# Optimization experiments

Hardware: AMD Instinct MI355X
Metric: run time of the kernel (lower is better)

## Reference

```python
import jax, jax.numpy as jnp
import numpy as np

LEAKY = 0.1

def _leaky(x):
    return jax.nn.leaky_relu(x, LEAKY)

def _gather(pts, idx):
    # pts: [B, M, C], idx: [B, N, K] -> [B, N, K, C]
    return jax.vmap(lambda p, i: p[i])(pts, idx)

def _cross(xyz1, xyz2, p1, p2, pos_w, pos_b, mlps, k):
    # xyz1:[B,N1,3] xyz2:[B,N2,3] p1:[B,N1,D] p2:[B,N2,D]
    d = (jnp.sum(xyz1 * xyz1, -1)[:, :, None]
         + jnp.sum(xyz2 * xyz2, -1)[:, None, :]
         - 2.0 * jnp.einsum('bnc,bmc->bnm', xyz1, xyz2))  # [B,N1,N2]
    _, idx = jax.lax.top_k(-d, k)                          # smallest-k -> [B,N1,K]
    nb_xyz = _gather(xyz2, idx)                            # [B,N1,K,3]
    direction = nb_xyz - xyz1[:, :, None, :]
    g2 = _gather(p2, idx)                                  # [B,N1,K,D]
    posf = direction @ pos_w.T + pos_b                     # 1x1 conv on 3->D
    x = _leaky(g2 + p1[:, :, None, :] + posf)              # bn = Identity
    for w, b in mlps:
        x = _leaky(x @ w.T + b)                            # 1x1 Conv2d + bias + leaky
    return jnp.max(x, axis=2)                              # max-pool over K -> [B,N1,Cout]

def setup_inputs() -> dict:
    key = jax.random.key(0)
    ks = jax.random.split(key, 24)
    B, N, C, M1, M2, K = 2, 8192, 64, 64, 64, 16
    s = 0.1
    inp = {
        'pc1': jax.random.normal(ks[0], (B, 3, N), jnp.float32),
        'pc2': jax.random.normal(ks[1], (B, 3, N), jnp.float32),
        'feat1': jax.random.normal(ks[2], (B, C, N), jnp.float32),
        'feat2': jax.random.normal(ks[3], (B, C, N), jnp.float32),
        't11_w': jax.random.normal(ks[4], (M1, C), jnp.float32) * s,
        't11_b': jax.random.normal(ks[5], (M1,), jnp.float32) * s,
        't22_w': jax.random.normal(ks[6], (M1, C), jnp.float32) * s,
        't22_b': jax.random.normal(ks[7], (M1,), jnp.float32) * s,
        'pos1_w': jax.random.normal(ks[8], (M1, 3), jnp.float32) * s,
        'pos1_b': jax.random.normal(ks[9], (M1,), jnp.float32) * s,
        'mlp1_w1': jax.random.normal(ks[10], (M1, M1), jnp.float32) * s,
        'mlp1_b1': jax.random.normal(ks[11], (M1,), jnp.float32) * s,
        'mlp1_w2': jax.random.normal(ks[12], (M1, M1), jnp.float32) * s,
        'mlp1_b2': jax.random.normal(ks[13], (M1,), jnp.float32) * s,
        't1_w': jax.random.normal(ks[14], (M2, M1), jnp.float32) * s,
        't1_b': jax.random.normal(ks[15], (M2,), jnp.float32) * s,
        't2_w': jax.random.normal(ks[16], (M2, M1), jnp.float32) * s,
        't2_b': jax.random.normal(ks[17], (M2,), jnp.float32) * s,
        'pos2_w': jax.random.normal(ks[18], (M2, 3), jnp.float32) * s,
        'pos2_b': jax.random.normal(ks[19], (M2,), jnp.float32) * s,
        'mlp2_w1': jax.random.normal(ks[20], (M2, M2), jnp.float32) * s,
        'mlp2_b1': jax.random.normal(ks[21], (M2,), jnp.float32) * s,
    }
    return inp

def reference(pc1, pc2, feat1, feat2,
              t11_w, t11_b, t22_w, t22_b,
              pos1_w, pos1_b, mlp1_w1, mlp1_b1, mlp1_w2, mlp1_b2,
              t1_w, t1_b, t2_w, t2_b,
              pos2_w, pos2_b, mlp2_w1, mlp2_b1):
    K = 16
    x1 = jnp.transpose(pc1, (0, 2, 1))    # [B,N,3]
    x2 = jnp.transpose(pc2, (0, 2, 1))
    f1 = jnp.transpose(feat1, (0, 2, 1))  # [B,N,C]
    f2 = jnp.transpose(feat2, (0, 2, 1))
    mlp1 = [(mlp1_w1, mlp1_b1), (mlp1_w2, mlp1_b2)]
    mlp2 = [(mlp2_w1, mlp2_b1)]
    # feat1_new = cross_t1(cross(pc1, pc2, t11(feat1), t22(feat2), pos1, mlp1))
    q1 = f1 @ t11_w.T + t11_b
    q2 = f2 @ t22_w.T + t22_b
    fn1 = _cross(x1, x2, q1, q2, pos1_w, pos1_b, mlp1, K) @ t1_w.T + t1_b  # [B,N,M2]
    # feat2_new = cross_t2(cross(pc2, pc1, t11(feat2), t22(feat1), pos1, mlp1))
    r1 = f2 @ t11_w.T + t11_b
    r2 = f1 @ t22_w.T + t22_b
    fn2 = _cross(x2, x1, r1, r2, pos1_w, pos1_b, mlp1, K) @ t2_w.T + t2_b  # [B,N,M2]
    # feat1_final = cross(pc1, pc2, feat1_new, feat2_new, pos2, mlp2)
    ff = _cross(x1, x2, fn1, fn2, pos2_w, pos2_b, mlp2, K)                 # [B,N,M2]
    to_cn = lambda a: jnp.transpose(a, (0, 2, 1))  # back to [B,C,N] torch layout
    return (to_cn(fn1), to_cn(fn2), to_cn(ff))
```

## Files before the change

kernel.cpp:

```cpp
#include <hip/hip_runtime.h>

#define NPTS 8192
#define BATCH 2
#define CC 64
#define KNN 16

typedef __attribute__((ext_vector_type(4))) float  f32x4;
typedef __attribute__((ext_vector_type(8))) short  s16x8;
typedef unsigned short u16;

__device__ __forceinline__ u16 f2bf(float f) {
  unsigned u = __float_as_uint(f);
  unsigned r = ((u >> 16) & 1u) + 0x7FFFu;
  return (u16)((u + r) >> 16);
}

__device__ __forceinline__ float leaky(float v) { return fmaxf(v, 0.1f * v); }

__device__ __forceinline__ s16x8 pack8(const float v[8]) {
  union { s16x8 v8; u16 s[8]; } u;
  #pragma unroll
  for (int j = 0; j < 8; ++j) u.s[j] = f2bf(v[j]);
  return u.v8;
}

__device__ __forceinline__ void split2(float v, u16& h, u16& l) {
  h = f2bf(v);
  float hf = __uint_as_float((unsigned)h << 16);
  l = f2bf(v - hf);
}

__global__ __launch_bounds__(256) void kprep(const float* __restrict__ pc1,
                                             const float* __restrict__ pc2,
                                             float4* __restrict__ x1t,
                                             float4* __restrict__ x2t,
                                             u16* __restrict__ arow1, u16* __restrict__ arow2,
                                             u16* __restrict__ brow1, u16* __restrict__ brow2) {
  int i = blockIdx.x * 256 + threadIdx.x;
  int b = i >> 13, n = i & (NPTS - 1);
  size_t base = (size_t)b * 3 * NPTS + n;
  #pragma unroll
  for (int c = 0; c < 2; ++c) {
    const float* pc = c ? pc2 : pc1;
    float4* xt = c ? x2t : x1t;
    u16* ar = c ? arow2 : arow1;
    u16* br = c ? brow2 : brow1;
    float x = pc[base], y = pc[base + NPTS], z = pc[base + 2 * NPTS];
    float w = x * x + y * y + z * z;
    xt[i] = make_float4(x, y, z, w);
    u16 A[32];
    #pragma unroll
    for (int j = 0; j < 32; ++j) A[j] = 0;
    u16 h, l;
    split2(-2.f * x, h, l); A[0] = h; A[1] = l; A[2] = h;
    split2(-2.f * y, h, l); A[3] = h; A[4] = l; A[5] = h;
    split2(-2.f * z, h, l); A[6] = h; A[7] = l; A[8] = h;
    split2(w, h, l);        A[9] = h; A[10] = l;
    A[11] = 0x3F80; A[12] = 0x3F80;
    uint4* ap = (uint4*)(ar + (size_t)i * 32);
    ap[0] = ((const uint4*)A)[0];
    ap[1] = ((const uint4*)A)[1];
    ap[2] = ((const uint4*)A)[2];
    ap[3] = ((const uint4*)A)[3];
    u16 Bv[16];
    #pragma unroll
    for (int j = 0; j < 16; ++j) Bv[j] = 0;
    split2(x, h, l); Bv[0] = h; Bv[1] = h; Bv[2] = l;
    split2(y, h, l); Bv[3] = h; Bv[4] = h; Bv[5] = l;
    split2(z, h, l); Bv[6] = h; Bv[7] = h; Bv[8] = l;
    Bv[9] = 0x3F80; Bv[10] = 0x3F80;
    split2(w, h, l); Bv[11] = h; Bv[12] = l;
    uint4* bp = (uint4*)(br + (size_t)i * 16);
    bp[0] = ((const uint4*)Bv)[0];
    bp[1] = ((const uint4*)Bv)[1];
  }
}

__global__ __launch_bounds__(256) void ktrans(
    const float* __restrict__ f1, const float* __restrict__ f2,
    const float* __restrict__ w11, const float* __restrict__ b11,
    const float* __restrict__ w22, const float* __restrict__ b22,
    float* __restrict__ q1, float* __restrict__ q2,
    float* __restrict__ r1, float* __restrict__ r2) {
  const int z = blockIdx.z;
  const float* in = (z == 0 || z == 3) ? f1 : f2;
  const float* W  = (z == 0 || z == 2) ? w11 : w22;
  const float* Bb = (z == 0 || z == 2) ? b11 : b22;
  float* out = (z == 0) ? q1 : (z == 1) ? q2 : (z == 2) ? r1 : r2;
  const int b = blockIdx.y;
  const int n0 = blockIdx.x * 64;
  const int t = threadIdx.x;

  __shared__ float ft[64 * 65];
  __shared__ float wt[64 * 68];

  #pragma unroll
  for (int j = 0; j < 16; ++j) {
    int e = t + 256 * j;
    int c = e >> 6, tn = e & 63;
    ft[c * 65 + tn] = in[((size_t)b * 64 + c) * NPTS + n0 + tn];
  }
  #pragma unroll
  for (int j = 0; j < 16; ++j) {
    int e = t + 256 * j;
    int mm = e >> 6, c = e & 63;
    wt[c * 68 + mm] = W[e];
  }
  __syncthreads();

  const int tn = t & 63, mg = t >> 6;
  float a[16];
  #pragma unroll
  for (int u = 0; u < 4; ++u) {
    float4 bb = *(const float4*)&Bb[16 * mg + 4 * u];
    a[4 * u] = bb.x; a[4 * u + 1] = bb.y; a[4 * u + 2] = bb.z; a[4 * u + 3] = bb.w;
  }
  for (int c = 0; c < 64; ++c) {
    float x = ft[c * 65 + tn];
    #pragma unroll
    for (int u = 0; u < 4; ++u) {
      float4 w4 = *(const float4*)&wt[c * 68 + 16 * mg + 4 * u];
      a[4 * u]     = fmaf(x, w4.x, a[4 * u]);
      a[4 * u + 1] = fmaf(x, w4.y, a[4 * u + 1]);
      a[4 * u + 2] = fmaf(x, w4.z, a[4 * u + 2]);
      a[4 * u + 3] = fmaf(x, w4.w, a[4 * u + 3]);
    }
  }
  size_t ob = ((size_t)b * NPTS + n0 + tn) * 64 + 16 * mg;
  #pragma unroll
  for (int u = 0; u < 4; ++u)
    *(float4*)&out[ob + 4 * u] =
        make_float4(a[4 * u], a[4 * u + 1], a[4 * u + 2], a[4 * u + 3]);
}

__device__ __forceinline__ void kinsert(unsigned key, unsigned ii,
                                        unsigned (&D)[16], unsigned (&I)[16]) {
  if (key < D[15]) {
    bool lt[16];
    #pragma unroll
    for (int j = 0; j < 16; ++j) lt[j] = key < D[j];
    #pragma unroll
    for (int j = 15; j >= 1; --j) {
      D[j] = lt[j - 1] ? D[j - 1] : (lt[j] ? key : D[j]);
      I[j] = lt[j - 1] ? I[j - 1] : (lt[j] ? ii  : I[j]);
    }
    if (lt[0]) { D[0] = key; I[0] = ii; }
  }
}

__device__ __forceinline__ void klex(unsigned key, unsigned ii,
                                     unsigned (&D)[16], unsigned (&I)[16]) {
  if ((key < D[15]) || (key == D[15] && ii < I[15])) {
    bool lt[16];
    #pragma unroll
    for (int j = 0; j < 16; ++j) lt[j] = (key < D[j]) || (key == D[j] && ii < I[j]);
    #pragma unroll
    for (int j = 15; j >= 1; --j) {
      D[j] = lt[j - 1] ? D[j - 1] : (lt[j] ? key : D[j]);
      I[j] = lt[j - 1] ? I[j - 1] : (lt[j] ? ii  : I[j]);
    }
    if (lt[0]) { D[0] = key; I[0] = ii; }
  }
}

#define CH 4
#define CKSZ (NPTS / CH)
#define RD 15
#define RT 11
#define FDELTA 0.008f
#define KINF 0x7F7FFFFFu

__global__ __launch_bounds__(256) void kknn(
    const float4* __restrict__ x1t, const float4* __restrict__ x2t,
    const u16* __restrict__ arow1, const u16* __restrict__ arow2,
    const u16* __restrict__ brow1, const u16* __restrict__ brow2,
    uint2* __restrict__ part) {
  const int dir = blockIdx.z;
  const int b = blockIdx.y;
  const float4* xq = dir ? x2t : x1t;
  const float4* xc = dir ? x1t : x2t;
  const u16* ar = dir ? arow1 : arow2;
  const u16* br = dir ? brow2 : brow1;
  const int t = threadIdx.x;
  const int lane = t & 63;
  const int w = t >> 6;
  const int m = lane & 15;
  const int kh = lane >> 4;
  const int qb = blockIdx.x & 127;
  const int ck = blockIdx.x >> 7;

  __shared__ float4 cxyz[CKSZ];
  __shared__ u16 ring[RD][256];

  const size_t cb = (size_t)b * NPTS + ck * CKSZ;
  #pragma unroll
  for (int j = 0; j < CKSZ / 256; ++j) cxyz[j * 256 + t] = xc[cb + j * 256 + t];

  const int qi = qb * 64 + w * 16 + m;
  const size_t qg = (size_t)b * NPTS + qi;
  float4 Q = xq[qg];
  const float nqx = -2.f * Q.x, nqy = -2.f * Q.y, nqz = -2.f * Q.z, qn = Q.w;

  s16x8 bf;
  if (kh < 2) bf = *(const s16x8*)(br + qg * 16 + kh * 8);
  else { s16x8 zb = {0,0,0,0,0,0,0,0}; bf = zb; }

  unsigned D[16], I[16];
  #pragma unroll
  for (int j = 0; j < 16; ++j) { D[j] = KINF; I[j] = 0u; }
  float tf = __uint_as_float(KINF);
  int cnt = 0;

  __syncthreads();

  const unsigned ibase = (unsigned)(ck * CKSZ);
  const u16* arb = ar + cb * 32;
  const f32x4 zz = {0.f, 0.f, 0.f, 0.f};

  s16x8 afC = *(const s16x8*)(arb + (size_t)m * 32 + kh * 8);

  for (int step = 0; step < CKSZ / 16; ++step) {
    s16x8 afN = *(const s16x8*)(arb + (size_t)((step + 1) * 16 + m) * 32 + kh * 8);
    f32x4 acc = __builtin_amdgcn_mfma_f32_16x16x32_bf16(afC, bf, zz, 0, 0, 0);
    int crow = step * 16 + kh * 4;
    #pragma unroll
    for (int r = 0; r < 4; ++r) {
      ring[cnt][t] = (u16)(crow + r);
      cnt += (acc[r] < tf) ? 1 : 0;
    }
    if (__any(cnt >= RT)) {
      for (int e = 0; e < cnt; ++e) {
        int ji = ring[e][t];
        float4 C = cxyz[ji];
        float d = fmaf(C.x, nqx, fmaf(C.y, nqy, fmaf(C.z, nqz, qn + C.w)));
        unsigned key = (unsigned)max((int)__float_as_uint(d), 0);
        kinsert(key, ibase + ji, D, I);
      }
      cnt = 0;
      unsigned s15 = min(D[15], (unsigned)__shfl_xor((int)D[15], 16));
      s15 = min(s15, (unsigned)__shfl_xor((int)s15, 32));
      s15 = min(s15, KINF);
      tf = __uint_as_float(s15) + FDELTA;
    }
    afC = afN;
  }
  for (int e = 0; e < cnt; ++e) {
    int ji = ring[e][t];
    float4 C = cxyz[ji];
    float d = fmaf(C.x, nqx, fmaf(C.y, nqy, fmaf(C.z, nqz, qn + C.w)));
    unsigned key = (unsigned)max((int)__float_as_uint(d), 0);
    kinsert(key, ibase + ji, D, I);
  }

  unsigned LD[16], LI[16];
  #pragma unroll
  for (int j = 0; j < 16; ++j) {
    unsigned od = (unsigned)__shfl_xor((int)D[15 - j], 16);
    unsigned oi = (unsigned)__shfl_xor((int)I[15 - j], 16);
    bool take = (D[j] < od) || (D[j] == od && I[j] < oi);
    LD[j] = take ? D[j] : od;
    LI[j] = take ? I[j] : oi;
  }
  #pragma unroll
  for (int dd = 8; dd >= 1; dd >>= 1) {
    #pragma unroll
    for (int j = 0; j < 16; ++j) {
      if (!(j & dd)) {
        int k2 = j + dd;
        bool sw = (LD[j] > LD[k2]) || (LD[j] == LD[k2] && LI[j] > LI[k2]);
        unsigned tk = LD[j], ti = LI[j];
        LD[j] = sw ? LD[k2] : LD[j];  LI[j] = sw ? LI[k2] : LI[j];
        LD[k2] = sw ? tk : LD[k2];    LI[k2] = sw ? ti : LI[k2];
      }
    }
  }
  unsigned MD[16], MI[16];
  #pragma unroll
  for (int j = 0; j < 16; ++j) {
    unsigned od = (unsigned)__shfl_xor((int)LD[15 - j], 32);
    unsigned oi = (unsigned)__shfl_xor((int)LI[15 - j], 32);
    bool take = (LD[j] < od) || (LD[j] == od && LI[j] < oi);
    MD[j] = take ? LD[j] : od;
    MI[j] = take ? LI[j] : oi;
  }
  if (kh == 0) {
    uint2* pb = part + ((size_t)((dir * 2 + b) * CH + ck) * 16) * NPTS;
    #pragma unroll
    for (int j = 0; j < 16; ++j)
      pb[(size_t)j * NPTS + qi] = make_uint2(MD[j], MI[j]);
  }
}

__global__ __launch_bounds__(256) void kmerge(const uint2* __restrict__ part,
                                              int* __restrict__ idx12,
                                              int* __restrict__ idx21) {
  const int dir = blockIdx.z, b = blockIdx.y;
  const int qi = blockIdx.x * 256 + threadIdx.x;
  const uint2* pb = part + ((size_t)((dir * 2 + b) * CH) * 16) * NPTS;

  unsigned D[16], I[16];
  #pragma unroll
  for (int j = 0; j < 16; ++j) { D[j] = KINF; I[j] = 0u; }
  for (int l = 0; l < CH; ++l) {
    #pragma unroll
    for (int j = 0; j < 16; ++j) {
      uint2 kv = pb[(size_t)(l * 16 + j) * NPTS + qi];
      klex(kv.x, kv.y, D, I);
    }
  }
  int* out = dir ? idx21 : idx12;
  size_t ob = ((size_t)b * NPTS + qi) * 16;
  #pragma unroll
  for (int j = 0; j < 16; ++j) out[ob + j] = (int)I[j];
}

template <int NL>
__global__ __launch_bounds__(256) void kcross(
    const float4* __restrict__ xq0, const float4* __restrict__ xc0, const int* __restrict__ idx0,
    const float* __restrict__ p10, const float* __restrict__ p20,
    float* __restrict__ orm0, float* __restrict__ ocn0,
    const float4* __restrict__ xq1, const float4* __restrict__ xc1, const int* __restrict__ idx1,
    const float* __restrict__ p11, const float* __restrict__ p21,
    float* __restrict__ orm1, float* __restrict__ ocn1,
    const float* __restrict__ posw, const float* __restrict__ posb,
    const float* __restrict__ w1, const float* __restrict__ b1,
    const float* __restrict__ w2, const float* __restrict__ b2) {
  const float4* xq; const float4* xc; const int* idx; const float* p1; const float* p2;
  float* orm; float* ocn;
  if (blockIdx.y == 0) { xq = xq0; xc = xc0; idx = idx0; p1 = p10; p2 = p20; orm = orm0; ocn = ocn0; }
  else                 { xq = xq1; xc = xc1; idx = idx1; p1 = p11; p2 = p21; orm = orm1; ocn = ocn1; }

  __shared__ float4 pw4[64];
  __shared__ __align__(16) u16 ylds[4][16 * 72];

  const int t = threadIdx.x;
  const int lane = t & 63;
  const int w = t >> 6;
  const int m = lane & 15;
  const int q = lane >> 4;

  if (t < 64) pw4[t] = make_float4(posw[t * 3], posw[t * 3 + 1], posw[t * 3 + 2], posb[t]);
  __syncthreads();

  s16x8 wf[2][4][2];
  float bv[2][4];
  #pragma unroll
  for (int l = 0; l < NL; ++l) {
    const float* Wl = l ? w2 : w1;
    const float* Bl = l ? b2 : b1;
    #pragma unroll
    for (int ct = 0; ct < 4; ++ct) {
      bv[l][ct] = Bl[16 * ct + m];
      const float* rowp = Wl + (size_t)(16 * ct + m) * 64;
      #pragma unroll
      for (int kt = 0; kt < 2; ++kt) {
        const float* pp = rowp + 32 * kt + 8 * q;
        float4 A  = *(const float4*)pp;
        float4 Bq = *(const float4*)(pp + 4);
        float vv[8] = {A.x, A.y, A.z, A.w, Bq.x, Bq.y, Bq.z, Bq.w};
        wf[l][ct][kt] = pack8(vv);
      }
    }
  }

  u16* yw = &ylds[w][0];
  const f32x4 zz = {0.f, 0.f, 0.f, 0.f};

  #pragma unroll 1
  for (int i = 0; i < 4; ++i) {
    int gp = blockIdx.x * 16 + w * 4 + i;
    int b = gp >> 13, n = gp & (NPTS - 1);
    size_t qb = (size_t)b * NPTS + n;
    int nb = idx[qb * 16 + m];
    size_t cb = (size_t)b * NPTS + nb;
    float4 qp  = xq[qb];
    float4 nbp = xc[cb];
    float dx = nbp.x - qp.x, dy = nbp.y - qp.y, dz = nbp.z - qp.z;

    s16x8 af[2];
    #pragma unroll
    for (int h = 0; h < 2; ++h) {
      int c0 = 32 * h + 8 * q;
      const float* g2p = p2 + cb * 64 + c0;
      float4 ga = *(const float4*)g2p;
      float4 gb = *(const float4*)(g2p + 4);
      const float* p1p = p1 + qb * 64 + c0;
      float4 pa = *(const float4*)p1p;
      float4 pb = *(const float4*)(p1p + 4);
      float gg[8] = {ga.x + pa.x, ga.y + pa.y, ga.z + pa.z, ga.w + pa.w,
                     gb.x + pb.x, gb.y + pb.y, gb.z + pb.z, gb.w + pb.w};
      float vv[8];
      #pragma unroll
      for (int j = 0; j < 8; ++j) {
        float4 pw = pw4[c0 + j];
        float v = gg[j] + pw.w;
        v = fmaf(dx, pw.x, v);
        v = fmaf(dy, pw.y, v);
        v = fmaf(dz, pw.z, v);
        vv[j] = leaky(v);
      }
      af[h] = pack8(vv);
    }

    f32x4 acc[4];
    #pragma unroll
    for (int ct = 0; ct < 4; ++ct) {
      acc[ct] = __builtin_amdgcn_mfma_f32_16x16x32_bf16(af[0], wf[0][ct][0], zz, 0, 0, 0);
      acc[ct] = __builtin_amdgcn_mfma_f32_16x16x32_bf16(af[1], wf[0][ct][1], acc[ct], 0, 0, 0);
    }
    float y[4][4];
    #pragma unroll
    for (int ct = 0; ct < 4; ++ct)
      #pragma unroll
      for (int r = 0; r < 4; ++r)
        y[ct][r] = leaky(acc[ct][r] + bv[0][ct]);

    if (NL == 2) {
      #pragma unroll
      for (int ct = 0; ct < 4; ++ct)
        #pragma unroll
        for (int r = 0; r < 4; ++r)
          yw[(q * 4 + r) * 72 + 16 * ct + m] = f2bf(y[ct][r]);
      asm volatile("s_waitcnt lgkmcnt(0)" ::: "memory");
      s16x8 a2[2];
      a2[0] = *(const s16x8*)(yw + m * 72 + 8 * q);
      a2[1] = *(const s16x8*)(yw + m * 72 + 32 + 8 * q);
      #pragma unroll
      for (int ct = 0; ct < 4; ++ct) {
        acc[ct] = __builtin_amdgcn_mfma_f32_16x16x32_bf16(a2[0], wf[1][ct][0], zz, 0, 0, 0);
        acc[ct] = __builtin_amdgcn_mfma_f32_16x16x32_bf16(a2[1], wf[1][ct][1], acc[ct], 0, 0, 0);
      }
      #pragma unroll
      for (int ct = 0; ct < 4; ++ct)
        #pragma unroll
        for (int r = 0; r < 4; ++r)
          y[ct][r] = leaky(acc[ct][r] + bv[1][ct]);
      asm volatile("s_waitcnt lgkmcnt(0)" ::: "memory");
    }

    float pm[4];
    #pragma unroll
    for (int ct = 0; ct < 4; ++ct) {
      float v = fmaxf(fmaxf(y[ct][0], y[ct][1]), fmaxf(y[ct][2], y[ct][3]));
      v = fmaxf(v, __shfl_xor(v, 16));
      v = fmaxf(v, __shfl_xor(v, 32));
      pm[ct] = v;
    }
    float sel = (q == 0) ? pm[0] : (q == 1) ? pm[1] : (q == 2) ? pm[2] : pm[3];
    if (orm) orm[qb * 64 + lane] = sel;
    if (ocn) ocn[((size_t)b * 64 + lane) * NPTS + n] = sel;
  }
}

__global__ __launch_bounds__(256) void kpost(
    const float* __restrict__ inA, const float* __restrict__ inB,
    const float* __restrict__ wA, const float* __restrict__ bA,
    const float* __restrict__ wB, const float* __restrict__ bB,
    float* __restrict__ frA, float* __restrict__ frB,
    float* __restrict__ cnA, float* __restrict__ cnB) {
  const int z = blockIdx.z;
  const float* in = z ? inB : inA;
  const float* W  = z ? wB : wA;
  const float* Bb = z ? bB : bA;
  float* fr = z ? frB : frA;
  float* cn = z ? cnB : cnA;
  const int b = blockIdx.y;
  const int n0 = blockIdx.x * 64;
  const int t = threadIdx.x;

  __shared__ float pl[64 * 65];
  __shared__ float wt[64 * 68];

  #pragma unroll
  for (int j = 0; j < 16; ++j) {
    int e = t + 256 * j;
    int r = e >> 6, c = e & 63;
    pl[r * 65 + c] = in[((size_t)b * NPTS + n0 + r) * 64 + c];
  }
  #pragma unroll
  for (int j = 0; j < 16; ++j) {
    int e = t + 256 * j;
    int mm = e >> 6, c = e & 63;
    wt[c * 68 + mm] = W[e];
  }
  __syncthreads();

  const int tn = t & 63, mg = t >> 6;
  float a[16];
  #pragma unroll
  for (int u = 0; u < 4; ++u) {
    float4 bb = *(const float4*)&Bb[16 * mg + 4 * u];
    a[4 * u] = bb.x; a[4 * u + 1] = bb.y; a[4 * u + 2] = bb.z; a[4 * u + 3] = bb.w;
  }
  for (int c = 0; c < 64; ++c) {
    float x = pl[tn * 65 + c];
    #pragma unroll
    for (int u = 0; u < 4; ++u) {
      float4 w4 = *(const float4*)&wt[c * 68 + 16 * mg + 4 * u];
      a[4 * u]     = fmaf(x, w4.x, a[4 * u]);
      a[4 * u + 1] = fmaf(x, w4.y, a[4 * u + 1]);
      a[4 * u + 2] = fmaf(x, w4.z, a[4 * u + 2]);
      a[4 * u + 3] = fmaf(x, w4.w, a[4 * u + 3]);
    }
  }
  size_t ob = ((size_t)b * NPTS + n0 + tn) * 64 + 16 * mg;
  #pragma unroll
  for (int u = 0; u < 4; ++u)
    *(float4*)&fr[ob + 4 * u] =
        make_float4(a[4 * u], a[4 * u + 1], a[4 * u + 2], a[4 * u + 3]);
  #pragma unroll
  for (int jj = 0; jj < 16; ++jj) {
    int mo = 16 * mg + jj;
    cn[((size_t)b * 64 + mo) * NPTS + n0 + tn] = a[jj];
  }
}

extern "C" void kernel_launch(void* const* d_in, const int* in_sizes, int n_in,
                              void* d_out, int out_size, void* d_ws, size_t ws_size,
                              hipStream_t stream) {
  const float* pc1   = (const float*)d_in[0];
  const float* pc2   = (const float*)d_in[1];
  const float* feat1 = (const float*)d_in[2];
  const float* feat2 = (const float*)d_in[3];
  const float* t11w  = (const float*)d_in[4];
  const float* t11b  = (const float*)d_in[5];
  const float* t22w  = (const float*)d_in[6];
  const float* t22b  = (const float*)d_in[7];
  const float* pos1w = (const float*)d_in[8];
  const float* pos1b = (const float*)d_in[9];
  const float* m1w1  = (const float*)d_in[10];
  const float* m1b1  = (const float*)d_in[11];
  const float* m1w2  = (const float*)d_in[12];
  const float* m1b2  = (const float*)d_in[13];
  const float* t1w   = (const float*)d_in[14];
  const float* t1b   = (const float*)d_in[15];
  const float* t2w   = (const float*)d_in[16];
  const float* t2b   = (const float*)d_in[17];
  const float* pos2w = (const float*)d_in[18];
  const float* pos2b = (const float*)d_in[19];
  const float* m2w1  = (const float*)d_in[20];
  const float* m2b1  = (const float*)d_in[21];

  char* ws = (char*)d_ws;
  size_t off = 0;
  auto take = [&](size_t bytes) {
    char* p = ws + off;
    off += (bytes + 255) & ~(size_t)255;
    return p;
  };
  float4* x1t  = (float4*)take((size_t)BATCH * NPTS * sizeof(float4));
  float4* x2t  = (float4*)take((size_t)BATCH * NPTS * sizeof(float4));
  int* idx12   = (int*)take((size_t)BATCH * NPTS * KNN * 4);
  int* idx21   = (int*)take((size_t)BATCH * NPTS * KNN * 4);
  u16* arow1   = (u16*)take(((size_t)BATCH * NPTS + 16) * 64);
  u16* arow2   = (u16*)take(((size_t)BATCH * NPTS + 16) * 64);
  u16* brow1   = (u16*)take((size_t)BATCH * NPTS * 32);
  u16* brow2   = (u16*)take((size_t)BATCH * NPTS * 32);
  float* q1    = (float*)take((size_t)BATCH * NPTS * CC * 4);
  float* q2    = (float*)take((size_t)BATCH * NPTS * CC * 4);
  float* r1    = (float*)take((size_t)BATCH * NPTS * CC * 4);
  float* r2    = (float*)take((size_t)BATCH * NPTS * CC * 4);
  float* poolA = (float*)take((size_t)BATCH * NPTS * CC * 4);
  float* poolB = (float*)take((size_t)BATCH * NPTS * CC * 4);
  float* fn1   = (float*)take((size_t)BATCH * NPTS * CC * 4);
  float* fn2   = (float*)take((size_t)BATCH * NPTS * CC * 4);
  uint2* part  = (uint2*)take((size_t)4 * CH * 16 * NPTS * sizeof(uint2));

  float* out = (float*)d_out;
  size_t seg = (size_t)BATCH * CC * NPTS;

  kprep<<<dim3(BATCH * NPTS / 256), 256, 0, stream>>>(
      pc1, pc2, x1t, x2t, arow1, arow2, brow1, brow2);
  kknn<<<dim3(128 * CH, BATCH, 2), 256, 0, stream>>>(
      x1t, x2t, arow1, arow2, brow1, brow2, part);
  kmerge<<<dim3(NPTS / 256, BATCH, 2), 256, 0, stream>>>(part, idx12, idx21);
  ktrans<<<dim3(NPTS / 64, BATCH, 4), 256, 0, stream>>>(
      feat1, feat2, t11w, t11b, t22w, t22b, q1, q2, r1, r2);
  kcross<2><<<dim3(1024, 2), 256, 0, stream>>>(
      x1t, x2t, idx12, q1, q2, poolA, (float*)nullptr,
      x2t, x1t, idx21, r1, r2, poolB, (float*)nullptr,
      pos1w, pos1b, m1w1, m1b1, m1w2, m1b2);
  kpost<<<dim3(NPTS / 64, BATCH, 2), 256, 0, stream>>>(
      poolA, poolB, t1w, t1b, t2w, t2b, fn1, fn2, out, out + seg);
  kcross<1><<<dim3(1024, 1), 256, 0, stream>>>(
      x1t, x2t, idx12, fn1, fn2, (float*)nullptr, out + 2 * seg,
      x1t, x2t, idx12, fn1, fn2, (float*)nullptr, (float*)nullptr,
      pos2w, pos2b, m2w1, m2b1, m2w1, m2b1);
}
```

Before: 517.7 us.

## Seed KNN threshold with exact scan of subset before MFMA-filtered remainder

The KNN search is split into two phases. The first kernel runs an exact scalar scan over the first 2048 candidates, in four 512-point subchunks, to get per-query top-16 lists. The second kernel takes the minimum 16th-distance across those lists, plus a margin, as its starting threshold for an MFMA-filtered scan of the remaining 6144 candidates. This should cut how many candidates get inserted, and it drops the cross-lane threshold sharing and the LDS candidate cache in favour of global loads. The merge now uses plain key inserts and seeds from the first list, the partial-list buffer is aliased onto the feature scratch buffers, and the final cross output is transposed through LDS so its channel-major writes are coalesced.

```diff
diff --git a/kernel.cpp b/kernel.cpp
--- a/kernel.cpp
+++ b/kernel.cpp
@@ -148,29 +148,79 @@
   }
 }
 
-__device__ __forceinline__ void klex(unsigned key, unsigned ii,
-                                     unsigned (&D)[16], unsigned (&I)[16]) {
-  if ((key < D[15]) || (key == D[15] && ii < I[15])) {
-    bool lt[16];
-    #pragma unroll
-    for (int j = 0; j < 16; ++j) lt[j] = (key < D[j]) || (key == D[j] && ii < I[j]);
-    #pragma unroll
-    for (int j = 15; j >= 1; --j) {
-      D[j] = lt[j - 1] ? D[j - 1] : (lt[j] ? key : D[j]);
-      I[j] = lt[j - 1] ? I[j - 1] : (lt[j] ? ii  : I[j]);
-    }
-    if (lt[0]) { D[0] = key; I[0] = ii; }
-  }
-}
-
-#define CH 4
-#define CKSZ (NPTS / CH)
-#define RD 15
-#define RT 11
-#define FDELTA 0.008f
-#define KINF 0x7F7FFFFFu
-
-__global__ __launch_bounds__(256) void kknn(
+#define ASUB 4
+#define ASZ 512
+#define WCK 3
+#define WCKSZ 2048
+#define NLISTS (ASUB + WCK)
+#define MARGIN 4e-3f
+
+#define ARD 24
+#define ART 16
+
+__global__ __launch_bounds__(256) void kknnA(const float4* __restrict__ x1t,
+                                             const float4* __restrict__ x2t,
+                                             uint2* __restrict__ part) {
+  const int dir = blockIdx.z;
+  const int b = blockIdx.y;
+  const float4* xq = dir ? x2t : x1t;
+  const float4* xc = dir ? x1t : x2t;
+  const int t = threadIdx.x;
+  const int qb = blockIdx.x & 31;
+  const int sc = blockIdx.x >> 5;
+  const int qi = qb * 256 + t;
+
+  __shared__ float4 tile[ASZ];
+  __shared__ uint2 ring[ARD][256];
+
+  const float4* src = xc + (size_t)b * NPTS + sc * ASZ;
+  #pragma unroll
+  for (int j = 0; j < ASZ / 256; ++j) tile[j * 256 + t] = src[j * 256 + t];
+
+  float4 Q = xq[(size_t)b * NPTS + qi];
+  const float nqx = -2.f * Q.x, nqy = -2.f * Q.y, nqz = -2.f * Q.z, qn = Q.w;
+
+  unsigned D[16], I[16];
+  #pragma unroll
+  for (int j = 0; j < 16; ++j) { D[j] = 0xFFFFFFFFu; I[j] = 0u; }
+  int cnt = 0;
+
+  __syncthreads();
+
+  const unsigned ibase = (unsigned)(sc * ASZ);
+  for (int j0 = 0; j0 < ASZ; j0 += 8) {
+    unsigned D15 = D[15];
+    #pragma unroll
+    for (int u = 0; u < 8; ++u) {
+      float4 C = tile[j0 + u];
+      float d = fmaf(C.x, nqx, fmaf(C.y, nqy, fmaf(C.z, nqz, qn + C.w)));
+      unsigned key = (unsigned)max((int)__float_as_uint(d), 0);
+      ring[cnt][t] = make_uint2(key, ibase + j0 + u);
+      cnt += (key < D15) ? 1 : 0;
+    }
+    if (__any(cnt >= ART)) {
+      for (int e = 0; e < cnt; ++e) {
+        uint2 kv = ring[e][t];
+        kinsert(kv.x, kv.y, D, I);
+      }
+      cnt = 0;
+    }
+  }
+  for (int e = 0; e < cnt; ++e) {
+    uint2 kv = ring[e][t];
+    kinsert(kv.x, kv.y, D, I);
+  }
+
+  uint2* pb = part + ((size_t)(((dir << 1) | b) * NLISTS + sc) * 16) * NPTS;
+  #pragma unroll
+  for (int j = 0; j < 16; ++j)
+    pb[(size_t)j * NPTS + qi] = make_uint2(D[j], I[j]);
+}
+
+#define MRD 24
+#define MRT 16
+
+__global__ __launch_bounds__(256) void kknnB(
     const float4* __restrict__ x1t, const float4* __restrict__ x2t,
     const u16* __restrict__ arow1, const u16* __restrict__ arow2,
     const u16* __restrict__ brow1, const u16* __restrict__ brow2,
@@ -189,13 +239,9 @@
   const int qb = blockIdx.x & 127;
   const int ck = blockIdx.x >> 7;
 
-  __shared__ float4 cxyz[CKSZ];
-  __shared__ u16 ring[RD][256];
-
-  const size_t cb = (size_t)b * NPTS + ck * CKSZ;
-  #pragma unroll
-  for (int j = 0; j < CKSZ / 256; ++j) cxyz[j * 256 + t] = xc[cb + j * 256 + t];
-
+  __shared__ u16 ring[MRD][256];
+
+  const int cbase = ASUB * ASZ + ck * WCKSZ;
   const int qi = qb * 64 + w * 16 + m;
   const size_t qg = (size_t)b * NPTS + qi;
   float4 Q = xq[qg];
@@ -205,21 +251,25 @@
   if (kh < 2) bf = *(const s16x8*)(br + qg * 16 + kh * 8);
   else { s16x8 zb = {0,0,0,0,0,0,0,0}; bf = zb; }
 
+  const size_t gb = (size_t)(((dir << 1) | b) * NLISTS) * 16 * NPTS;
+  unsigned tm = part[gb + (size_t)15 * NPTS + qi].x;
+  #pragma unroll
+  for (int s = 1; s < ASUB; ++s)
+    tm = min(tm, part[gb + (size_t)(s * 16 + 15) * NPTS + qi].x);
+  float tf = __uint_as_float(tm) + MARGIN;
+
   unsigned D[16], I[16];
   #pragma unroll
-  for (int j = 0; j < 16; ++j) { D[j] = KINF; I[j] = 0u; }
-  float tf = __uint_as_float(KINF);
+  for (int j = 0; j < 16; ++j) { D[j] = 0xFFFFFFFFu; I[j] = 0u; }
   int cnt = 0;
 
-  __syncthreads();
-
-  const unsigned ibase = (unsigned)(ck * CKSZ);
+  const size_t cb = (size_t)b * NPTS + cbase;
   const u16* arb = ar + cb * 32;
   const f32x4 zz = {0.f, 0.f, 0.f, 0.f};
 
   s16x8 afC = *(const s16x8*)(arb + (size_t)m * 32 + kh * 8);
 
-  for (int step = 0; step < CKSZ / 16; ++step) {
+  for (int step = 0; step < WCKSZ / 16; ++step) {
     s16x8 afN = *(const s16x8*)(arb + (size_t)((step + 1) * 16 + m) * 32 + kh * 8);
     f32x4 acc = __builtin_amdgcn_mfma_f32_16x16x32_bf16(afC, bf, zz, 0, 0, 0);
     int crow = step * 16 + kh * 4;
@@ -228,28 +278,25 @@
       ring[cnt][t] = (u16)(crow + r);
       cnt += (acc[r] < tf) ? 1 : 0;
     }
-    if (__any(cnt >= RT)) {
+    if (__any(cnt >= MRT)) {
       for (int e = 0; e < cnt; ++e) {
         int ji = ring[e][t];
-        float4 C = cxyz[ji];
+        float4 C = xc[cb + ji];
         float d = fmaf(C.x, nqx, fmaf(C.y, nqy, fmaf(C.z, nqz, qn + C.w)));
         unsigned key = (unsigned)max((int)__float_as_uint(d), 0);
-        kinsert(key, ibase + ji, D, I);
+        kinsert(key, (unsigned)(cbase + ji), D, I);
       }
       cnt = 0;
-      unsigned s15 = min(D[15], (unsigned)__shfl_xor((int)D[15], 16));
-      s15 = min(s15, (unsigned)__shfl_xor((int)s15, 32));
-      s15 = min(s15, KINF);
-      tf = __uint_as_float(s15) + FDELTA;
+      tf = fminf(tf, __uint_as_float(D[15]) + MARGIN);
     }
     afC = afN;
   }
   for (int e = 0; e < cnt; ++e) {
     int ji = ring[e][t];
-    float4 C = cxyz[ji];
+    float4 C = xc[cb + ji];
     float d = fmaf(C.x, nqx, fmaf(C.y, nqy, fmaf(C.z, nqz, qn + C.w)));
     unsigned key = (unsigned)max((int)__float_as_uint(d), 0);
-    kinsert(key, ibase + ji, D, I);
+    kinsert(key, (unsigned)(cbase + ji), D, I);
   }
 
   unsigned LD[16], LI[16];
@@ -284,7 +331,7 @@
     MI[j] = take ? LI[j] : oi;
   }
   if (kh == 0) {
-    uint2* pb = part + ((size_t)((dir * 2 + b) * CH + ck) * 16) * NPTS;
+    uint2* pb = part + ((size_t)(((dir << 1) | b) * NLISTS + ASUB + ck) * 16) * NPTS;
     #pragma unroll
     for (int j = 0; j < 16; ++j)
       pb[(size_t)j * NPTS + qi] = make_uint2(MD[j], MI[j]);
@@ -296,16 +343,19 @@
                                               int* __restrict__ idx21) {
   const int dir = blockIdx.z, b = blockIdx.y;
   const int qi = blockIdx.x * 256 + threadIdx.x;
-  const uint2* pb = part + ((size_t)((dir * 2 + b) * CH) * 16) * NPTS;
+  const uint2* pb = part + ((size_t)(((dir << 1) | b) * NLISTS) * 16) * NPTS;
 
   unsigned D[16], I[16];
   #pragma unroll
-  for (int j = 0; j < 16; ++j) { D[j] = KINF; I[j] = 0u; }
-  for (int l = 0; l < CH; ++l) {
+  for (int j = 0; j < 16; ++j) {
+    uint2 kv = pb[(size_t)j * NPTS + qi];
+    D[j] = kv.x; I[j] = kv.y;
+  }
+  for (int l = 1; l < NLISTS; ++l) {
     #pragma unroll
     for (int j = 0; j < 16; ++j) {
       uint2 kv = pb[(size_t)(l * 16 + j) * NPTS + qi];
-      klex(kv.x, kv.y, D, I);
+      kinsert(kv.x, kv.y, D, I);
     }
   }
   int* out = dir ? idx21 : idx12;
@@ -332,6 +382,7 @@
 
   __shared__ float4 pw4[64];
   __shared__ __align__(16) u16 ylds[4][16 * 72];
+  __shared__ float otile[16][68];
 
   const int t = threadIdx.x;
   const int lane = t & 63;
@@ -448,7 +499,18 @@
     }
     float sel = (q == 0) ? pm[0] : (q == 1) ? pm[1] : (q == 2) ? pm[2] : pm[3];
     if (orm) orm[qb * 64 + lane] = sel;
-    if (ocn) ocn[((size_t)b * 64 + lane) * NPTS + n] = sel;
+    if (ocn) otile[w * 4 + i][lane] = sel;
+  }
+
+  if (ocn) {
+    __syncthreads();
+    int gp0 = blockIdx.x * 16;
+    int b = gp0 >> 13, n0 = gp0 & (NPTS - 1);
+    int ch = t >> 2;
+    int nn = (t & 3) * 4;
+    float4 v = make_float4(otile[nn][ch], otile[nn + 1][ch],
+                           otile[nn + 2][ch], otile[nn + 3][ch]);
+    *(float4*)&ocn[((size_t)b * 64 + ch) * NPTS + n0 + nn] = v;
   }
 }
 
@@ -564,14 +626,15 @@
   float* poolB = (float*)take((size_t)BATCH * NPTS * CC * 4);
   float* fn1   = (float*)take((size_t)BATCH * NPTS * CC * 4);
   float* fn2   = (float*)take((size_t)BATCH * NPTS * CC * 4);
-  uint2* part  = (uint2*)take((size_t)4 * CH * 16 * NPTS * sizeof(uint2));
+  uint2* part  = (uint2*)q1;
 
   float* out = (float*)d_out;
   size_t seg = (size_t)BATCH * CC * NPTS;
 
   kprep<<<dim3(BATCH * NPTS / 256), 256, 0, stream>>>(
       pc1, pc2, x1t, x2t, arow1, arow2, brow1, brow2);
-  kknn<<<dim3(128 * CH, BATCH, 2), 256, 0, stream>>>(
+  kknnA<<<dim3(32 * ASUB, BATCH, 2), 256, 0, stream>>>(x1t, x2t, part);
+  kknnB<<<dim3(128 * WCK, BATCH, 2), 256, 0, stream>>>(
       x1t, x2t, arow1, arow2, brow1, brow2, part);
   kmerge<<<dim3(NPTS / 256, BATCH, 2), 256, 0, stream>>>(part, idx12, idx21);
   ktrans<<<dim3(NPTS / 64, BATCH, 4), 256, 0, stream>>>(
```

Result: faster. 469.2 us (-9.4%).
